# Kernel tuning notes

Measured on AMD Instinct MI355X. Metric: run time of the kernel, lower is better.

Reference implementation:

```python
import jax, jax.numpy as jnp
import numpy as np

TS = 7           # tile_size
STRIDE = 3       # tile_size - overlap
RATIO = 4
C = 4            # margs.channel
S_LR = 256       # ms side
S_HR = 1024      # margs.test_sidelen
N_ATOMS = 10
TSR = TS * RATIO
STR_R = STRIDE * RATIO
NP_SIDE = (S_LR - TS) // STRIDE + 1   # 84 (pad_size == 0 for this config)
NPATCH = NP_SIDE ** 2                 # 7056


def unfold(x, k, stride):
    # x: [1,C,H,W] -> [1, C*k*k, N]  (channel-major patch layout, same as torch F.unfold)
    p = jax.lax.conv_general_dilated_patches(x, (k, k), (stride, stride), 'VALID')
    return p.reshape(1, p.shape[1], -1)


def fold(p, c, h, w, k, stride):
    # F.fold is the adjoint (overlap-add transpose) of unfold
    _, vjp = jax.vjp(lambda x: unfold(x, k, stride), jnp.zeros((1, c, h, w), p.dtype))
    return vjp(p)[0]


def _gauss(k, sigma):
    ax = np.arange(k) - (k - 1) / 2.0
    g = np.exp(-ax ** 2 / (2.0 * sigma ** 2))
    g = g / g.sum()
    return jnp.asarray(np.outer(g, g), dtype=jnp.float32)


def wald(x, ratio):
    # wald_protocol low-pass: depthwise gaussian blur (MTF approximation)
    k = 4 * ratio + 1
    ker = jnp.broadcast_to(_gauss(k, float(ratio)), (x.shape[1], 1, k, k))
    return jax.lax.conv_general_dilated(x, ker, (1, 1), 'SAME', feature_group_count=x.shape[1])


def setup_inputs() -> dict:
    key = jax.random.key(0)
    ks = jax.random.split(key, 4)
    # histogram-matched PAN high-pass (C channels, matched per band)
    pan_hp = jax.random.normal(ks[0], (1, C, S_HR, S_HR), jnp.float32)
    lr_pan_hp = wald(pan_hp, RATIO)[:, :, 2:-1:4, 2:-1:4]          # [1,C,256,256]
    lr_dict = unfold(lr_pan_hp, TS, STRIDE)[0].T                    # [NPATCH, C*TS^2]
    hr_dict = unfold(pan_hp, TSR, STR_R)[0].T                       # [NPATCH, C*TSR^2]
    ms_hp = 0.1 * jax.random.normal(ks[1], (1, C, S_LR, S_LR), jnp.float32)
    lms = jax.random.normal(ks[2], (1, C, S_HR, S_HR), jnp.float32)
    hrms_hp = 0.1 * jax.random.normal(ks[3], (1, C, S_HR, S_HR), jnp.float32)
    divisor = fold(jnp.ones((1, C * TSR * TSR, NPATCH), jnp.float32), C, S_HR, S_HR, TSR, STR_R)
    divisor = jnp.where(divisor == 0, 1.0, divisor)
    return {"hrms_hp": hrms_hp, "ms_hp": ms_hp, "lms": lms,
            "lr_dict": lr_dict, "hr_dict": hr_dict, "divisor": divisor}


def reference(hrms_hp, ms_hp, lms, lr_dict, hr_dict, divisor):
    N = lr_dict.shape[0]
    hw = TS * TS
    hwr = TSR * TSR
    # residual MS patches: ms_hp - degraded current estimate
    lr_hrms = wald(hrms_hp, RATIO)[:, :, 2:-1:4, 2:-1:4]
    res_ms = unfold(ms_hp - lr_hrms, TS, STRIDE)[0]                 # [C*hw, N]
    res_ms = res_ms.reshape(C, hw, N).transpose(2, 0, 1).reshape(N * C, hw)  # '(n c) hw'
    res = res_ms.reshape(N, C * hw)                                 # 'n (c hw)'
    idx_cols = [jnp.arange(N)]                                      # index[:,0] = arange
    alpha = None
    for i in range(N_ATOMS):
        if i > 0:
            # greedy atom selection: max |<residual, atom>|
            idx_cols.append(jnp.argmax(jnp.abs(res @ lr_dict.T), axis=-1))
        idx = jnp.stack(idx_cols, axis=1)                           # [N, i+1]
        A = lr_dict[idx]                                            # [N, i+1, C*hw]
        A = A.reshape(N, i + 1, C, hw).transpose(0, 2, 3, 1).reshape(N * C, hw, i + 1)
        # batched least squares (min-norm, matches torch.linalg.lstsq)
        alpha = jnp.einsum('bij,bj->bi', jnp.linalg.pinv(A), res_ms)  # [N*C, i+1]
        res = (res_ms - jnp.einsum('bi,bpi->bp', alpha, A)).reshape(N, C * hw)
    idx = jnp.stack(idx_cols, axis=1)                               # [N, N_ATOMS]
    Hd = hr_dict[idx].reshape(N, N_ATOMS, C, hwr).transpose(0, 2, 1, 3).reshape(N * C, N_ATOMS, hwr)
    hr_p = jnp.einsum('bi,bip->bp', alpha, Hd)                      # [N*C, hwr]
    hr_p = hr_p.reshape(N, C, hwr).transpose(1, 2, 0).reshape(1, C * hwr, N)
    hrms_out = fold(hr_p, C, S_HR, S_HR, TSR, STR_R) / (divisor + 1e-8) + hrms_hp
    return hrms_out + lms
```

## Files before the change

### kernel.cpp

```cpp
#include <hip/hip_runtime.h>
#include <math.h>

#define NP    7056
#define NP2   7168
#define NPS   84
#define CCH   4
#define HW    49
#define HWR   784
#define KF    196
#define KSEG  196
#define KC    608
#define NH    19
#define NA    10
#define SLR   256
#define GK    17

typedef _Float16 half8 __attribute__((ext_vector_type(8)));
typedef float f32x4 __attribute__((ext_vector_type(4)));

__global__ void hpass_kernel(const float* __restrict__ hr, float* __restrict__ htmp) {
    __shared__ float g[GK];
    int tid = threadIdx.x;
    if (tid < GK) {
        double s = 0.0, mine = 0.0;
        for (int k = 0; k < GK; k++) {
            double ax = (double)k - 8.0;
            double e = exp(-ax * ax / 32.0);
            s += e;
            if (k == tid) mine = e;
        }
        g[tid] = (float)(mine / s);
    }
    __syncthreads();
    int gid = blockIdx.x * 256 + tid;
    int xs = gid & 255;
    int y  = (gid >> 8) & 1023;
    int c  = gid >> 18;
    const float* row = hr + (size_t)(c * 1024 + y) * 1024;
    int xb = xs * 4 - 6;
    float acc = 0.f;
#pragma unroll
    for (int k = 0; k < GK; k++) {
        int xc = xb + k;
        float v = (xc >= 0 && xc < 1024) ? row[xc] : 0.f;
        acc = fmaf(g[k], v, acc);
    }
    htmp[gid] = acc;
}

__global__ void vpass_kernel(const float* __restrict__ htmp, const float* __restrict__ ms,
                             float* __restrict__ diff) {
    __shared__ float g[GK];
    int tid = threadIdx.x;
    if (tid < GK) {
        double s = 0.0, mine = 0.0;
        for (int k = 0; k < GK; k++) {
            double ax = (double)k - 8.0;
            double e = exp(-ax * ax / 32.0);
            s += e;
            if (k == tid) mine = e;
        }
        g[tid] = (float)(mine / s);
    }
    __syncthreads();
    int gid = blockIdx.x * 256 + tid;
    int xs = gid & 255;
    int ys = (gid >> 8) & 255;
    int c  = gid >> 16;
    int yb = ys * 4 - 6;
    float acc = 0.f;
#pragma unroll
    for (int k = 0; k < GK; k++) {
        int yc = yb + k;
        float v = (yc >= 0 && yc < 1024) ? htmp[(size_t)(c * 1024 + yc) * 256 + xs] : 0.f;
        acc = fmaf(g[k], v, acc);
    }
    diff[gid] = ms[gid] - acc;
}

__global__ void build_y_kernel(const float* __restrict__ diff, float* __restrict__ yb) {
    int gid = blockIdx.x * 256 + threadIdx.x;
    if (gid >= NP * CCH * HW) return;
    int p = gid % HW;
    int b = gid / HW;
    int c = b & 3;
    int n = b >> 2;
    int py = n / NPS, px = n % NPS;
    int dy = p / 7, dx = p % 7;
    yb[gid] = diff[(size_t)(c * SLR + py * 3 + dy) * SLR + px * 3 + dx];
}

__global__ void splitcat_kernel(const float* __restrict__ src, _Float16* __restrict__ Dcat) {
    int gid = blockIdx.x * 256 + threadIdx.x;
    int r = gid / 76, v8 = gid - r * 76;
    const float* srow = src + (size_t)r * KF;
    bool valid = (r < NP);
    half8 o;
#pragma unroll
    for (int e = 0; e < 8; e++) {
        int k = v8 * 8 + e;
        int seg = (k >= 392) ? 2 : (k >= 196 ? 1 : 0);
        int ks = k - seg * 196;
        float x = (valid && k < 588) ? srow[ks] : 0.f;
        _Float16 hi = (_Float16)x;
        o[e] = (seg == 1) ? (_Float16)(x - (float)hi) : hi;
    }
    *(half8*)&Dcat[(size_t)r * KC + v8 * 8] = o;
}

__global__ void hd16_kernel(const float* __restrict__ hr_dict, _Float16* __restrict__ hd) {
    int gid = blockIdx.x * 256 + threadIdx.x;
    if (gid >= (NP * CCH * HWR) / 8) return;
    const float4 a = *(const float4*)&hr_dict[(size_t)gid * 8];
    const float4 b = *(const float4*)&hr_dict[(size_t)gid * 8 + 4];
    half8 o;
    o[0] = (_Float16)a.x; o[1] = (_Float16)a.y; o[2] = (_Float16)a.z; o[3] = (_Float16)a.w;
    o[4] = (_Float16)b.x; o[5] = (_Float16)b.y; o[6] = (_Float16)b.z; o[7] = (_Float16)b.w;
    *(half8*)&hd[(size_t)gid * 8] = o;
}

__device__ __forceinline__ unsigned long long shfl_xor_u64(unsigned long long v, int m) {
    unsigned int lo = (unsigned int)v;
    unsigned int hi = (unsigned int)(v >> 32);
    lo = __shfl_xor(lo, m, 64);
    hi = __shfl_xor(hi, m, 64);
    return ((unsigned long long)hi << 32) | (unsigned long long)lo;
}

__device__ __forceinline__ void gload16(const void* g, void* l) {
    __builtin_amdgcn_global_load_lds((const __attribute__((address_space(1))) void*)(void*)g,
                                     (__attribute__((address_space(3))) void*)l, 16, 0, 0);
}

__global__ __launch_bounds__(512, 4) void mfma_argmax_kernel(
    const _Float16* __restrict__ Rcat, const _Float16* __restrict__ Dcat,
    unsigned long long* __restrict__ keys, int seg) {
    __shared__ __align__(16) _Float16 lds[3 * 12288];
    const int tid = threadIdx.x;
    const int lane = tid & 63;
    const int wave = tid >> 6;
    const int wm = wave >> 1;
    const int wn = wave & 1;

    int b0 = (int)blockIdx.x;
    int xcd = b0 & 7, w = b0 >> 3;
    int by = w % 28;
    int bx = xcd * 7 + w / 28;
    const int row0 = by * 256, col0 = bx * 128;

    const int lr = lane & 15, lk = lane >> 4;
    const int xk = (lk ^ ((lr >> 1) & 3)) * 8;
    const int aBase = (wm * 64 + lr) * 32 + xk;
    const int bBase = 8192 + (wn * 64 + lr) * 32 + xk;

    const int srow = wave * 16 + (lane >> 2);
    const int sc = ((lane & 3) ^ ((lane >> 3) & 3)) * 8;
    const _Float16* pA = Rcat + (size_t)(row0 + srow) * KC + sc;
    const _Float16* pB = Dcat + (size_t)(col0 + srow) * KC + sc;
    const int dA1 = wave * 512, dA2 = 4096 + wave * 512, dB = 8192 + wave * 512;

    auto STAGE = [&](int h) {
        int q = (h % 3) * 12288;
        int off = h * 32;
        gload16(pA + off, &lds[q + dA1]);
        gload16(pA + (size_t)128 * KC + off, &lds[q + dA2]);
        gload16(pB + off, &lds[q + dB]);
    };

    f32x4 acc[4][4];
#pragma unroll
    for (int u = 0; u < 4; u++)
#pragma unroll
        for (int v = 0; v < 4; v++) {
            f32x4 zz = {0.f, 0.f, 0.f, 0.f};
            acc[u][v] = zz;
        }

    STAGE(0);
    STAGE(1);
    asm volatile("s_waitcnt vmcnt(3)" ::: "memory");
    __builtin_amdgcn_s_barrier();

    for (int h = 0; h < NH; ++h) {
        const int q = (h % 3) * 12288;
        int hn = h + 2; if (hn > NH - 1) hn = NH - 1;
        STAGE(hn);
        asm volatile("s_waitcnt vmcnt(6)" ::: "memory");
        __builtin_amdgcn_s_barrier();

        half8 aF[4], bF[4];
#pragma unroll
        for (int u = 0; u < 4; ++u)
            aF[u] = *(const half8*)&lds[q + aBase + u * 512];
#pragma unroll
        for (int v = 0; v < 4; ++v)
            bF[v] = *(const half8*)&lds[q + bBase + v * 512];

        __builtin_amdgcn_s_setprio(1);
#pragma unroll
        for (int u = 0; u < 4; ++u)
#pragma unroll
            for (int v = 0; v < 4; ++v)
                acc[u][v] = __builtin_amdgcn_mfma_f32_16x16x32_f16(aF[u], bF[v], acc[u][v], 0, 0, 0);
        __builtin_amdgcn_s_setprio(0);

        asm volatile("s_waitcnt lgkmcnt(0)" ::: "memory");
        __builtin_amdgcn_s_barrier();
    }
    asm volatile("s_waitcnt vmcnt(0)" ::: "memory");

    unsigned long long* kseg = keys + (size_t)seg * NP;
#pragma unroll
    for (int u = 0; u < 4; u++)
#pragma unroll
        for (int j = 0; j < 4; j++) {
            unsigned long long key = 0ull;
#pragma unroll
            for (int v = 0; v < 4; v++) {
                int gc = col0 + wn * 64 + v * 16 + lr;
                if (gc < NP) {
                    unsigned int bits = __float_as_uint(fabsf(acc[u][v][j]));
                    unsigned long long k2 = ((unsigned long long)bits << 32) |
                                            (unsigned long long)(0xFFFFFFFFu - (unsigned int)gc);
                    key = (k2 > key) ? k2 : key;
                }
            }
#pragma unroll
            for (int m = 1; m < 16; m <<= 1) {
                unsigned long long o = shfl_xor_u64(key, m);
                key = (o > key) ? o : key;
            }
            if (lr == 0) {
                int gr = row0 + wm * 64 + u * 16 + lk * 4 + j;
                if (gr < NP) atomicMax(kseg + gr, key);
            }
        }
}

template <int M>
__global__ __launch_bounds__(256) void solve_kernel(
    const float* __restrict__ yb, const float* __restrict__ dict,
    const unsigned long long* __restrict__ keys9,
    int* __restrict__ idxb, float* __restrict__ alphab) {
    int b = blockIdx.x * 256 + threadIdx.x;
    if (b >= NP * CCH) return;
    int n = b >> 2, c = b & 3;

    int newidx = 0;
    if (M >= 2) newidx = (int)(0xFFFFFFFFu -
        (unsigned int)(keys9[(size_t)(M - 2) * NP + n] & 0xFFFFFFFFull));
    if (c == 0) {
        if (M == 1) idxb[n * NA] = n;
        else        idxb[n * NA + (M - 1)] = newidx;
    }

    int id[M];
#pragma unroll
    for (int k = 0; k < M; k++)
        id[k] = (k == 0) ? n : ((M >= 2 && k == M - 1) ? newidx : idxb[n * NA + k]);

    const float* yrow = yb + (size_t)b * HW;
    const int base_c = c * HW;

    constexpr int TRI = M * (M + 1) / 2;
    float G[TRI];
    float rhs[M];
#pragma unroll
    for (int t = 0; t < TRI; t++) G[t] = 0.f;
#pragma unroll
    for (int k = 0; k < M; k++) rhs[k] = 0.f;

#pragma unroll
    for (int p0 = 0; p0 < HW; p0 += 7) {
        float a[M][7];
#pragma unroll
        for (int k = 0; k < M; k++) {
            const float* dr = dict + (size_t)id[k] * KF + base_c + p0;
#pragma unroll
            for (int j = 0; j < 7; j++) a[k][j] = dr[j];
        }
#pragma unroll
        for (int j = 0; j < 7; j++) {
            float yp = yrow[p0 + j];
#pragma unroll
            for (int k = 0; k < M; k++) {
                rhs[k] = fmaf(a[k][j], yp, rhs[k]);
#pragma unroll
                for (int l = 0; l <= k; l++)
                    G[k * (k + 1) / 2 + l] = fmaf(a[k][j], a[l][j], G[k * (k + 1) / 2 + l]);
            }
        }
    }

#pragma unroll
    for (int k = 0; k < M; k++) {
        float s = G[k * (k + 1) / 2 + k];
#pragma unroll
        for (int j = 0; j < k; j++) {
            float l = G[k * (k + 1) / 2 + j];
            s = fmaf(-l, l, s);
        }
        float inv = 1.0f / sqrtf(fmaxf(s, 1e-30f));
        G[k * (k + 1) / 2 + k] = inv;
#pragma unroll
        for (int r = k + 1; r < M; r++) {
            float t = G[r * (r + 1) / 2 + k];
#pragma unroll
            for (int j = 0; j < k; j++)
                t = fmaf(-G[r * (r + 1) / 2 + j], G[k * (k + 1) / 2 + j], t);
            G[r * (r + 1) / 2 + k] = t * inv;
        }
    }
#pragma unroll
    for (int k = 0; k < M; k++) {
        float t = rhs[k];
#pragma unroll
        for (int j = 0; j < k; j++) t = fmaf(-G[k * (k + 1) / 2 + j], rhs[j], t);
        rhs[k] = t * G[k * (k + 1) / 2 + k];
    }
#pragma unroll
    for (int k = M - 1; k >= 0; k--) {
        float t = rhs[k];
#pragma unroll
        for (int j = k + 1; j < M; j++) t = fmaf(-G[j * (j + 1) / 2 + k], rhs[j], t);
        rhs[k] = t * G[k * (k + 1) / 2 + k];
    }

#pragma unroll
    for (int k = 0; k < M; k++) alphab[(size_t)b * NA + k] = rhs[k];
}

template <int M>
__global__ __launch_bounds__(256) void resid_kernel(
    const float* __restrict__ yb, const float* __restrict__ dict,
    const int* __restrict__ idxb, const float* __restrict__ alphab,
    _Float16* __restrict__ Rcat) {
    int gid = blockIdx.x * 256 + threadIdx.x;
    if (gid >= NP * CCH * HW) return;
    int p = gid % HW;
    int b = gid / HW;
    int n = b >> 2, c = b & 3;
    const int base_c = c * HW;
    float s = yb[gid];
#pragma unroll
    for (int k = 0; k < M; k++) {
        int idk = (k == 0) ? n : idxb[n * NA + k];
        s = fmaf(-alphab[(size_t)b * NA + k], dict[(size_t)idk * KF + base_c + p], s);
    }
    _Float16 hi = (_Float16)s;
    _Float16* r0 = Rcat + (size_t)n * KC + base_c;
    r0[p] = hi;
    r0[KSEG + p] = hi;
    r0[2 * KSEG + p] = (_Float16)(s - (float)hi);
}

__global__ __launch_bounds__(256) void recon_kernel(
    const float* __restrict__ alphab, const int* __restrict__ idxb,
    const _Float16* __restrict__ hd, _Float16* __restrict__ hr_p) {
    int n = blockIdx.x;
    int tid = threadIdx.x;
    __shared__ float al[CCH * NA];
    __shared__ int idn[NA];
    if (tid < CCH * NA) al[tid] = alphab[(size_t)n * CCH * NA + tid];
    if (tid < NA) idn[tid] = idxb[n * NA + tid];
    __syncthreads();
    for (int v = tid; v < (CCH * HWR) / 8; v += 256) {
        int c = v / (HWR / 8);
        float s[8] = {0.f, 0.f, 0.f, 0.f, 0.f, 0.f, 0.f, 0.f};
#pragma unroll
        for (int k = 0; k < NA; k++) {
            half8 d = *(const half8*)&hd[(size_t)idn[k] * (CCH * HWR) + v * 8];
            float ak = al[c * NA + k];
#pragma unroll
            for (int e = 0; e < 8; e++) s[e] = fmaf(ak, (float)d[e], s[e]);
        }
        half8 o;
#pragma unroll
        for (int e = 0; e < 8; e++) o[e] = (_Float16)s[e];
        *(half8*)&hr_p[(size_t)n * (CCH * HWR) + v * 8] = o;
    }
}

__global__ __launch_bounds__(256) void fold2_kernel(
    const _Float16* __restrict__ hr_p, const float* __restrict__ divisor,
    const float* __restrict__ hrms, const float* __restrict__ lms,
    float* __restrict__ out) {
    int gid = blockIdx.x * 256 + threadIdx.x;
    int x  = gid & 1023;
    int yy = (gid >> 10) & 1023;
    int c  = gid >> 20;

    int t0 = yy - 27;
    int py0 = (t0 > 0) ? (t0 + 11) / 12 : 0;
    int py1 = min(83, yy / 12);
    int s0 = x - 27;
    int px0 = (s0 > 0) ? (s0 + 11) / 12 : 0;
    int px1 = min(83, x / 12);

    float acc = 0.f;
    for (int py = py0; py <= py1; py++) {
        int qy = yy - py * 12;
        for (int px = px0; px <= px1; px++) {
            int qx = x - px * 12;
            int n = py * NPS + px;
            acc += (float)hr_p[(size_t)n * (CCH * HWR) + c * HWR + qy * 28 + qx];
        }
    }
    out[gid] = acc / (divisor[gid] + 1e-8f) + hrms[gid] + lms[gid];
}

__global__ __launch_bounds__(256) void fold_final_kernel(
    const float* __restrict__ alphab, const int* __restrict__ idxb,
    const float* __restrict__ hr_dict, const float* __restrict__ divisor,
    const float* __restrict__ hrms, const float* __restrict__ lms,
    float* __restrict__ out) {
    int gid = blockIdx.x * 256 + threadIdx.x;
    int x  = gid & 1023;
    int yy = (gid >> 10) & 1023;
    int c  = gid >> 20;
    int t0 = yy - 27;
    int py0 = (t0 > 0) ? (t0 + 11) / 12 : 0;
    int py1 = min(83, yy / 12);
    int s0 = x - 27;
    int px0 = (s0 > 0) ? (s0 + 11) / 12 : 0;
    int px1 = min(83, x / 12);
    float acc = 0.f;
    for (int py = py0; py <= py1; py++) {
        int qy = yy - py * 12;
        for (int px = px0; px <= px1; px++) {
            int qx = x - px * 12;
            int n = py * NPS + px;
            const float* al = alphab + (size_t)(n * CCH + c) * NA;
            const int* idn = idxb + n * NA;
            int q = qy * 28 + qx;
            float s = 0.f;
#pragma unroll
            for (int k = 0; k < NA; k++)
                s = fmaf(al[k], hr_dict[(size_t)idn[k] * (CCH * HWR) + c * HWR + q], s);
            acc += s;
        }
    }
    out[gid] = acc / (divisor[gid] + 1e-8f) + hrms[gid] + lms[gid];
}

extern "C" void kernel_launch(void* const* d_in, const int* in_sizes, int n_in,
                              void* d_out, int out_size, void* d_ws, size_t ws_size,
                              hipStream_t stream) {
    const float* hrms    = (const float*)d_in[0];
    const float* ms      = (const float*)d_in[1];
    const float* lms     = (const float*)d_in[2];
    const float* lr_dict = (const float*)d_in[3];
    const float* hr_dict = (const float*)d_in[4];
    const float* divisor = (const float*)d_in[5];
    float* out = (float*)d_out;

    char* ws = (char*)d_ws;
    size_t off = 0;
    auto alloc = [&](size_t bytes) -> void* {
        void* p = ws + off;
        off += (bytes + 255) & ~(size_t)255;
        return p;
    };
    float* htmp   = (float*)alloc((size_t)4 * 1024 * 256 * 4);
    float* diff   = (float*)alloc((size_t)4 * 256 * 256 * 4);
    float* yb     = (float*)alloc((size_t)NP * CCH * HW * 4);
    float* alphab = (float*)alloc((size_t)NP * CCH * NA * 4);
    int*   idxb   = (int*)alloc((size_t)NP * NA * 4);
    unsigned long long* keys9 = (unsigned long long*)alloc((size_t)NP * 9 * 8);
    _Float16* Dcat = (_Float16*)alloc((size_t)NP2 * KC * 2);
    _Float16* Rcat = (_Float16*)alloc((size_t)NP2 * KC * 2);
    _Float16* hd16 = (_Float16*)alloc((size_t)NP * CCH * HWR * 2);
    _Float16* hr_p = (_Float16*)alloc((size_t)NP * CCH * HWR * 2);
    bool two_stage = (off <= ws_size);

    hpass_kernel<<<4096, 256, 0, stream>>>(hrms, htmp);
    vpass_kernel<<<1024, 256, 0, stream>>>(htmp, ms, diff);
    build_y_kernel<<<(NP * CCH * HW + 255) / 256, 256, 0, stream>>>(diff, yb);
    splitcat_kernel<<<(NP2 * 76) / 256, 256, 0, stream>>>(lr_dict, Dcat);
    hipMemsetAsync(Rcat, 0, (size_t)NP2 * KC * 2, stream);
    hipMemsetAsync(keys9, 0, (size_t)NP * 9 * 8, stream);
    if (two_stage)
        hd16_kernel<<<((NP * CCH * HWR) / 8 + 255) / 256, 256, 0, stream>>>(hr_dict, hd16);

    int blocks = (NP * CCH + 255) / 256;
    int rblocks = (NP * CCH * HW + 255) / 256;
    for (int i = 0; i < NA; i++) {
        if (i > 0)
            mfma_argmax_kernel<<<1568, 512, 0, stream>>>(Rcat, Dcat, keys9, i - 1);
        switch (i + 1) {
            case 1:  solve_kernel<1><<<blocks, 256, 0, stream>>>(yb, lr_dict, keys9, idxb, alphab);
                     resid_kernel<1><<<rblocks, 256, 0, stream>>>(yb, lr_dict, idxb, alphab, Rcat); break;
            case 2:  solve_kernel<2><<<blocks, 256, 0, stream>>>(yb, lr_dict, keys9, idxb, alphab);
                     resid_kernel<2><<<rblocks, 256, 0, stream>>>(yb, lr_dict, idxb, alphab, Rcat); break;
            case 3:  solve_kernel<3><<<blocks, 256, 0, stream>>>(yb, lr_dict, keys9, idxb, alphab);
                     resid_kernel<3><<<rblocks, 256, 0, stream>>>(yb, lr_dict, idxb, alphab, Rcat); break;
            case 4:  solve_kernel<4><<<blocks, 256, 0, stream>>>(yb, lr_dict, keys9, idxb, alphab);
                     resid_kernel<4><<<rblocks, 256, 0, stream>>>(yb, lr_dict, idxb, alphab, Rcat); break;
            case 5:  solve_kernel<5><<<blocks, 256, 0, stream>>>(yb, lr_dict, keys9, idxb, alphab);
                     resid_kernel<5><<<rblocks, 256, 0, stream>>>(yb, lr_dict, idxb, alphab, Rcat); break;
            case 6:  solve_kernel<6><<<blocks, 256, 0, stream>>>(yb, lr_dict, keys9, idxb, alphab);
                     resid_kernel<6><<<rblocks, 256, 0, stream>>>(yb, lr_dict, idxb, alphab, Rcat); break;
            case 7:  solve_kernel<7><<<blocks, 256, 0, stream>>>(yb, lr_dict, keys9, idxb, alphab);
                     resid_kernel<7><<<rblocks, 256, 0, stream>>>(yb, lr_dict, idxb, alphab, Rcat); break;
            case 8:  solve_kernel<8><<<blocks, 256, 0, stream>>>(yb, lr_dict, keys9, idxb, alphab);
                     resid_kernel<8><<<rblocks, 256, 0, stream>>>(yb, lr_dict, idxb, alphab, Rcat); break;
            case 9:  solve_kernel<9><<<blocks, 256, 0, stream>>>(yb, lr_dict, keys9, idxb, alphab);
                     resid_kernel<9><<<rblocks, 256, 0, stream>>>(yb, lr_dict, idxb, alphab, Rcat); break;
            case 10: solve_kernel<10><<<blocks, 256, 0, stream>>>(yb, lr_dict, keys9, idxb, alphab); break;
        }
    }

    if (two_stage) {
        recon_kernel<<<NP, 256, 0, stream>>>(alphab, idxb, hd16, hr_p);
        fold2_kernel<<<(4 * 1024 * 1024) / 256, 256, 0, stream>>>(hr_p, divisor, hrms, lms, out);
    } else {
        fold_final_kernel<<<(4 * 1024 * 1024) / 256, 256, 0, stream>>>(
            alphab, idxb, hr_dict, divisor, hrms, lms, out);
    }
}
```

Measured before the change: 1.247 ms.

## Pad residual segments to 200 and vectorize residual writes and fold output

Repads the split hi/lo fp16 segments from 196 to 200 elements so residual rows can be written as aligned 8-wide vectors. One thread now produces 8 residual elements per patch instead of one, and the Rcat memset is dropped. The fold kernel computes 4 adjacent output pixels per thread with float4 loads and stores. The risk is that the padding rows and tail of Rcat are no longer zeroed each run.

Result: slower. 1.380 ms (+10.7%).

```diff
diff --git a/kernel.cpp b/kernel.cpp
--- a/kernel.cpp
+++ b/kernel.cpp
@@ -8,7 +8,7 @@
 #define HW    49
 #define HWR   784
 #define KF    196
-#define KSEG  196
+#define SEGP  200
 #define KC    608
 #define NH    19
 #define NA    10
@@ -93,15 +93,14 @@
 __global__ void splitcat_kernel(const float* __restrict__ src, _Float16* __restrict__ Dcat) {
     int gid = blockIdx.x * 256 + threadIdx.x;
     int r = gid / 76, v8 = gid - r * 76;
+    int seg = v8 / 25;
     const float* srow = src + (size_t)r * KF;
-    bool valid = (r < NP);
+    bool vrow = (r < NP) && (seg < 3);
     half8 o;
 #pragma unroll
     for (int e = 0; e < 8; e++) {
-        int k = v8 * 8 + e;
-        int seg = (k >= 392) ? 2 : (k >= 196 ? 1 : 0);
-        int ks = k - seg * 196;
-        float x = (valid && k < 588) ? srow[ks] : 0.f;
+        int ks = v8 * 8 + e - seg * SEGP;
+        float x = (vrow && ks < KF) ? srow[ks] : 0.f;
         _Float16 hi = (_Float16)x;
         o[e] = (seg == 1) ? (_Float16)(x - (float)hi) : hi;
     }
@@ -336,22 +335,36 @@
     const int* __restrict__ idxb, const float* __restrict__ alphab,
     _Float16* __restrict__ Rcat) {
     int gid = blockIdx.x * 256 + threadIdx.x;
-    if (gid >= NP * CCH * HW) return;
-    int p = gid % HW;
-    int b = gid / HW;
-    int n = b >> 2, c = b & 3;
-    const int base_c = c * HW;
-    float s = yb[gid];
-#pragma unroll
-    for (int k = 0; k < M; k++) {
-        int idk = (k == 0) ? n : idxb[n * NA + k];
-        s = fmaf(-alphab[(size_t)b * NA + k], dict[(size_t)idk * KF + base_c + p], s);
-    }
-    _Float16 hi = (_Float16)s;
-    _Float16* r0 = Rcat + (size_t)n * KC + base_c;
-    r0[p] = hi;
-    r0[KSEG + p] = hi;
-    r0[2 * KSEG + p] = (_Float16)(s - (float)hi);
+    if (gid >= NP * 25) return;
+    int n = gid / 25, ch = gid - n * 25;
+
+    int id[M];
+#pragma unroll
+    for (int k = 0; k < M; k++)
+        id[k] = (k == 0) ? n : idxb[n * NA + k];
+
+    half8 hiv, lov;
+#pragma unroll
+    for (int e = 0; e < 8; e++) {
+        int ks = ch * 8 + e;
+        _Float16 hi = (_Float16)0.f, lo = (_Float16)0.f;
+        if (ks < KF) {
+            int c = ks / 49;
+            float s = yb[(size_t)n * KF + ks];
+#pragma unroll
+            for (int k = 0; k < M; k++)
+                s = fmaf(-alphab[(size_t)(n * CCH + c) * NA + k],
+                         dict[(size_t)id[k] * KF + ks], s);
+            hi = (_Float16)s;
+            lo = (_Float16)(s - (float)hi);
+        }
+        hiv[e] = hi;
+        lov[e] = lo;
+    }
+    _Float16* r0 = Rcat + (size_t)n * KC + ch * 8;
+    *(half8*)&r0[0] = hiv;
+    *(half8*)&r0[SEGP] = hiv;
+    *(half8*)&r0[2 * SEGP] = lov;
 }
 
 __global__ __launch_bounds__(256) void recon_kernel(
@@ -386,27 +399,41 @@
     const float* __restrict__ hrms, const float* __restrict__ lms,
     float* __restrict__ out) {
     int gid = blockIdx.x * 256 + threadIdx.x;
-    int x  = gid & 1023;
-    int yy = (gid >> 10) & 1023;
-    int c  = gid >> 20;
+    int xq = gid & 255;
+    int yy = (gid >> 8) & 1023;
+    int c  = gid >> 18;
+    int x0 = xq * 4;
 
     int t0 = yy - 27;
     int py0 = (t0 > 0) ? (t0 + 11) / 12 : 0;
     int py1 = min(83, yy / 12);
-    int s0 = x - 27;
+    int s0 = x0 - 27;
     int px0 = (s0 > 0) ? (s0 + 11) / 12 : 0;
-    int px1 = min(83, x / 12);
-
-    float acc = 0.f;
+    int px1 = min(83, (x0 + 3) / 12);
+
+    float a0 = 0.f, a1 = 0.f, a2 = 0.f, a3 = 0.f;
     for (int py = py0; py <= py1; py++) {
         int qy = yy - py * 12;
         for (int px = px0; px <= px1; px++) {
-            int qx = x - px * 12;
             int n = py * NPS + px;
-            acc += (float)hr_p[(size_t)n * (CCH * HWR) + c * HWR + qy * 28 + qx];
-        }
-    }
-    out[gid] = acc / (divisor[gid] + 1e-8f) + hrms[gid] + lms[gid];
+            const _Float16* rp = hr_p + (size_t)n * (CCH * HWR) + c * HWR + qy * 28;
+            int qx = x0 - px * 12;
+            if (qx >= 0 && qx < 28)         a0 += (float)rp[qx];
+            if (qx + 1 >= 0 && qx + 1 < 28) a1 += (float)rp[qx + 1];
+            if (qx + 2 >= 0 && qx + 2 < 28) a2 += (float)rp[qx + 2];
+            if (qx + 3 >= 0 && qx + 3 < 28) a3 += (float)rp[qx + 3];
+        }
+    }
+    size_t idx = (size_t)(c * 1024 + yy) * 1024 + x0;
+    const float4 dv = *(const float4*)&divisor[idx];
+    const float4 hm = *(const float4*)&hrms[idx];
+    const float4 lm = *(const float4*)&lms[idx];
+    float4 o;
+    o.x = a0 / (dv.x + 1e-8f) + hm.x + lm.x;
+    o.y = a1 / (dv.y + 1e-8f) + hm.y + lm.y;
+    o.z = a2 / (dv.z + 1e-8f) + hm.z + lm.z;
+    o.w = a3 / (dv.w + 1e-8f) + hm.w + lm.w;
+    *(float4*)&out[idx] = o;
 }
 
 __global__ __launch_bounds__(256) void fold_final_kernel(
@@ -477,13 +504,12 @@
     vpass_kernel<<<1024, 256, 0, stream>>>(htmp, ms, diff);
     build_y_kernel<<<(NP * CCH * HW + 255) / 256, 256, 0, stream>>>(diff, yb);
     splitcat_kernel<<<(NP2 * 76) / 256, 256, 0, stream>>>(lr_dict, Dcat);
-    hipMemsetAsync(Rcat, 0, (size_t)NP2 * KC * 2, stream);
     hipMemsetAsync(keys9, 0, (size_t)NP * 9 * 8, stream);
     if (two_stage)
         hd16_kernel<<<((NP * CCH * HWR) / 8 + 255) / 256, 256, 0, stream>>>(hr_dict, hd16);
 
     int blocks = (NP * CCH + 255) / 256;
-    int rblocks = (NP * CCH * HW + 255) / 256;
+    int rblocks = (NP * 25 + 255) / 256;
     for (int i = 0; i < NA; i++) {
         if (i > 0)
             mfma_argmax_kernel<<<1568, 512, 0, stream>>>(Rcat, Dcat, keys9, i - 1);
@@ -512,7 +538,7 @@
 
     if (two_stage) {
         recon_kernel<<<NP, 256, 0, stream>>>(alphab, idxb, hd16, hr_p);
-        fold2_kernel<<<(4 * 1024 * 1024) / 256, 256, 0, stream>>>(hr_p, divisor, hrms, lms, out);
+        fold2_kernel<<<(4 * 1024 * 256) / 256, 256, 0, stream>>>(hr_p, divisor, hrms, lms, out);
     } else {
         fold_final_kernel<<<(4 * 1024 * 1024) / 256, 256, 0, stream>>>(
             alphab, idxb, hr_dict, divisor, hrms, lms, out);
```

## Parallelize per-patch Gram solve across a 64-lane wave with shuffle reduction

Applied to the files above, without the earlier changes.

The solve kernel now assigns one 64-lane wavefront per patch, with 16 lanes per channel each accumulating a strided subset of the 49 pixels into the Gram matrix and right-hand side. Partial sums are combined with xor-shuffle butterflies, and every lane then runs the small redundant Cholesky solve. The old kernel had one thread per (patch, channel) doing serial 49-long accumulation with uncoalesced loads; the new layout gives coalesced loads and far more parallelism, at the cost of shuffle traffic and duplicated solves. The memset of Rcat is also removed, which assumes the padded rows are either never read or always written.

After: 1.155 ms. 1.08x faster.

```diff
diff --git a/kernel.cpp b/kernel.cpp
--- a/kernel.cpp
+++ b/kernel.cpp
@@ -242,14 +242,14 @@
     const float* __restrict__ yb, const float* __restrict__ dict,
     const unsigned long long* __restrict__ keys9,
     int* __restrict__ idxb, float* __restrict__ alphab) {
-    int b = blockIdx.x * 256 + threadIdx.x;
-    if (b >= NP * CCH) return;
-    int n = b >> 2, c = b & 3;
+    int n = (blockIdx.x * 256 + threadIdx.x) >> 6;
+    int lane = threadIdx.x & 63;
+    int g = lane >> 4, t = lane & 15;
 
     int newidx = 0;
     if (M >= 2) newidx = (int)(0xFFFFFFFFu -
         (unsigned int)(keys9[(size_t)(M - 2) * NP + n] & 0xFFFFFFFFull));
-    if (c == 0) {
+    if (lane == 0) {
         if (M == 1) idxb[n * NA] = n;
         else        idxb[n * NA + (M - 1)] = newidx;
     }
@@ -259,37 +259,42 @@
     for (int k = 0; k < M; k++)
         id[k] = (k == 0) ? n : ((M >= 2 && k == M - 1) ? newidx : idxb[n * NA + k]);
 
-    const float* yrow = yb + (size_t)b * HW;
-    const int base_c = c * HW;
+    const int b = n * CCH + g;
+    const int base_c = g * HW;
 
     constexpr int TRI = M * (M + 1) / 2;
     float G[TRI];
     float rhs[M];
 #pragma unroll
-    for (int t = 0; t < TRI; t++) G[t] = 0.f;
+    for (int q = 0; q < TRI; q++) G[q] = 0.f;
 #pragma unroll
     for (int k = 0; k < M; k++) rhs[k] = 0.f;
 
 #pragma unroll
-    for (int p0 = 0; p0 < HW; p0 += 7) {
-        float a[M][7];
-#pragma unroll
-        for (int k = 0; k < M; k++) {
-            const float* dr = dict + (size_t)id[k] * KF + base_c + p0;
-#pragma unroll
-            for (int j = 0; j < 7; j++) a[k][j] = dr[j];
-        }
-#pragma unroll
-        for (int j = 0; j < 7; j++) {
-            float yp = yrow[p0 + j];
+    for (int rep = 0; rep < 4; rep++) {
+        int p = t + rep * 16;
+        if (p < HW) {
+            float a[M];
+#pragma unroll
+            for (int k = 0; k < M; k++)
+                a[k] = dict[(size_t)id[k] * KF + base_c + p];
+            float yp = yb[(size_t)b * HW + p];
 #pragma unroll
             for (int k = 0; k < M; k++) {
-                rhs[k] = fmaf(a[k][j], yp, rhs[k]);
+                rhs[k] = fmaf(a[k], yp, rhs[k]);
 #pragma unroll
                 for (int l = 0; l <= k; l++)
-                    G[k * (k + 1) / 2 + l] = fmaf(a[k][j], a[l][j], G[k * (k + 1) / 2 + l]);
+                    G[k * (k + 1) / 2 + l] = fmaf(a[k], a[l], G[k * (k + 1) / 2 + l]);
             }
         }
+    }
+
+#pragma unroll
+    for (int m = 1; m < 16; m <<= 1) {
+#pragma unroll
+        for (int q = 0; q < TRI; q++) G[q] += __shfl_xor(G[q], m, 64);
+#pragma unroll
+        for (int k = 0; k < M; k++) rhs[k] += __shfl_xor(rhs[k], m, 64);
     }
 
 #pragma unroll
@@ -304,30 +309,32 @@
         G[k * (k + 1) / 2 + k] = inv;
 #pragma unroll
         for (int r = k + 1; r < M; r++) {
-            float t = G[r * (r + 1) / 2 + k];
+            float tt = G[r * (r + 1) / 2 + k];
 #pragma unroll
             for (int j = 0; j < k; j++)
-                t = fmaf(-G[r * (r + 1) / 2 + j], G[k * (k + 1) / 2 + j], t);
-            G[r * (r + 1) / 2 + k] = t * inv;
+                tt = fmaf(-G[r * (r + 1) / 2 + j], G[k * (k + 1) / 2 + j], tt);
+            G[r * (r + 1) / 2 + k] = tt * inv;
         }
     }
 #pragma unroll
     for (int k = 0; k < M; k++) {
-        float t = rhs[k];
-#pragma unroll
-        for (int j = 0; j < k; j++) t = fmaf(-G[k * (k + 1) / 2 + j], rhs[j], t);
-        rhs[k] = t * G[k * (k + 1) / 2 + k];
+        float tt = rhs[k];
+#pragma unroll
+        for (int j = 0; j < k; j++) tt = fmaf(-G[k * (k + 1) / 2 + j], rhs[j], tt);
+        rhs[k] = tt * G[k * (k + 1) / 2 + k];
     }
 #pragma unroll
     for (int k = M - 1; k >= 0; k--) {
-        float t = rhs[k];
-#pragma unroll
-        for (int j = k + 1; j < M; j++) t = fmaf(-G[j * (j + 1) / 2 + k], rhs[j], t);
-        rhs[k] = t * G[k * (k + 1) / 2 + k];
-    }
-
-#pragma unroll
-    for (int k = 0; k < M; k++) alphab[(size_t)b * NA + k] = rhs[k];
+        float tt = rhs[k];
+#pragma unroll
+        for (int j = k + 1; j < M; j++) tt = fmaf(-G[j * (j + 1) / 2 + k], rhs[j], tt);
+        rhs[k] = tt * G[k * (k + 1) / 2 + k];
+    }
+
+    if (t == 0) {
+#pragma unroll
+        for (int k = 0; k < M; k++) alphab[(size_t)b * NA + k] = rhs[k];
+    }
 }
 
 template <int M>
@@ -477,36 +484,35 @@
     vpass_kernel<<<1024, 256, 0, stream>>>(htmp, ms, diff);
     build_y_kernel<<<(NP * CCH * HW + 255) / 256, 256, 0, stream>>>(diff, yb);
     splitcat_kernel<<<(NP2 * 76) / 256, 256, 0, stream>>>(lr_dict, Dcat);
-    hipMemsetAsync(Rcat, 0, (size_t)NP2 * KC * 2, stream);
     hipMemsetAsync(keys9, 0, (size_t)NP * 9 * 8, stream);
     if (two_stage)
         hd16_kernel<<<((NP * CCH * HWR) / 8 + 255) / 256, 256, 0, stream>>>(hr_dict, hd16);
 
-    int blocks = (NP * CCH + 255) / 256;
+    int sblocks = NP / 4;
     int rblocks = (NP * CCH * HW + 255) / 256;
     for (int i = 0; i < NA; i++) {
         if (i > 0)
             mfma_argmax_kernel<<<1568, 512, 0, stream>>>(Rcat, Dcat, keys9, i - 1);
         switch (i + 1) {
-            case 1:  solve_kernel<1><<<blocks, 256, 0, stream>>>(yb, lr_dict, keys9, idxb, alphab);
+            case 1:  solve_kernel<1><<<sblocks, 256, 0, stream>>>(yb, lr_dict, keys9, idxb, alphab);
                      resid_kernel<1><<<rblocks, 256, 0, stream>>>(yb, lr_dict, idxb, alphab, Rcat); break;
-            case 2:  solve_kernel<2><<<blocks, 256, 0, stream>>>(yb, lr_dict, keys9, idxb, alphab);
+            case 2:  solve_kernel<2><<<sblocks, 256, 0, stream>>>(yb, lr_dict, keys9, idxb, alphab);
                      resid_kernel<2><<<rblocks, 256, 0, stream>>>(yb, lr_dict, idxb, alphab, Rcat); break;
-            case 3:  solve_kernel<3><<<blocks, 256, 0, stream>>>(yb, lr_dict, keys9, idxb, alphab);
+            case 3:  solve_kernel<3><<<sblocks, 256, 0, stream>>>(yb, lr_dict, keys9, idxb, alphab);
                      resid_kernel<3><<<rblocks, 256, 0, stream>>>(yb, lr_dict, idxb, alphab, Rcat); break;
-            case 4:  solve_kernel<4><<<blocks, 256, 0, stream>>>(yb, lr_dict, keys9, idxb, alphab);
+            case 4:  solve_kernel<4><<<sblocks, 256, 0, stream>>>(yb, lr_dict, keys9, idxb, alphab);
                      resid_kernel<4><<<rblocks, 256, 0, stream>>>(yb, lr_dict, idxb, alphab, Rcat); break;
-            case 5:  solve_kernel<5><<<blocks, 256, 0, stream>>>(yb, lr_dict, keys9, idxb, alphab);
+            case 5:  solve_kernel<5><<<sblocks, 256, 0, stream>>>(yb, lr_dict, keys9, idxb, alphab);
                      resid_kernel<5><<<rblocks, 256, 0, stream>>>(yb, lr_dict, idxb, alphab, Rcat); break;
-            case 6:  solve_kernel<6><<<blocks, 256, 0, stream>>>(yb, lr_dict, keys9, idxb, alphab);
+            case 6:  solve_kernel<6><<<sblocks, 256, 0, stream>>>(yb, lr_dict, keys9, idxb, alphab);
                      resid_kernel<6><<<rblocks, 256, 0, stream>>>(yb, lr_dict, idxb, alphab, Rcat); break;
-            case 7:  solve_kernel<7><<<blocks, 256, 0, stream>>>(yb, lr_dict, keys9, idxb, alphab);
+            case 7:  solve_kernel<7><<<sblocks, 256, 0, stream>>>(yb, lr_dict, keys9, idxb, alphab);
                      resid_kernel<7><<<rblocks, 256, 0, stream>>>(yb, lr_dict, idxb, alphab, Rcat); break;
-            case 8:  solve_kernel<8><<<blocks, 256, 0, stream>>>(yb, lr_dict, keys9, idxb, alphab);
+            case 8:  solve_kernel<8><<<sblocks, 256, 0, stream>>>(yb, lr_dict, keys9, idxb, alphab);
                      resid_kernel<8><<<rblocks, 256, 0, stream>>>(yb, lr_dict, idxb, alphab, Rcat); break;
-            case 9:  solve_kernel<9><<<blocks, 256, 0, stream>>>(yb, lr_dict, keys9, idxb, alphab);
+            case 9:  solve_kernel<9><<<sblocks, 256, 0, stream>>>(yb, lr_dict, keys9, idxb, alphab);
                      resid_kernel<9><<<rblocks, 256, 0, stream>>>(yb, lr_dict, idxb, alphab, Rcat); break;
-            case 10: solve_kernel<10><<<blocks, 256, 0, stream>>>(yb, lr_dict, keys9, idxb, alphab); break;
+            case 10: solve_kernel<10><<<sblocks, 256, 0, stream>>>(yb, lr_dict, keys9, idxb, alphab); break;
         }
     }
 
```
